# Kernel tuning notes

Measured on AMD Instinct MI355X. Metric: run time of the kernel, lower is better.

Reference implementation:

```python
import jax, jax.numpy as jnp
import numpy as np

N = 50000          # total nodes
E = 800000         # edges (avg degree 16)
IN = 128           # in_feat
HID = 64           # hidden per head
HEADS = (4, 4, 1)
NEG_SLOPE = 0.2    # DGL GATConv leaky_relu default


def setup_inputs() -> dict:
    key = jax.random.key(0)
    ks = jax.random.split(key, 16)

    def w(k, shape, fan_in):
        return jax.random.normal(k, shape, jnp.float32) / np.float32(np.sqrt(fan_in))

    inp = {
        "feat": jax.random.normal(ks[0], (N, IN), jnp.float32),
        "src": jax.random.randint(ks[1], (E,), 0, N, jnp.int32),
        "dst": jax.random.randint(ks[2], (E,), 0, N, jnp.int32),
    }
    dims = [(IN, HEADS[0]), (HID * HEADS[0], HEADS[1]), (HID * HEADS[1], HEADS[2])]
    j = 3
    for i, (din, h) in enumerate(dims, 1):
        inp[f"W{i}"] = w(ks[j], (din, h * HID), din); j += 1
        inp[f"al{i}"] = w(ks[j], (h, HID), HID); j += 1
        inp[f"ar{i}"] = w(ks[j], (h, HID), HID); j += 1
        inp[f"b{i}"] = jnp.zeros((h * HID,), jnp.float32)
    return inp


def gat_layer(x, W, al, ar, b, src, dst, n_heads):
    # DGL GATConv: linear -> per-node attn logits -> edge leaky_relu ->
    # per-dst segment softmax -> weighted scatter-sum -> + bias
    h = (x @ W).reshape(N, n_heads, HID)                     # [N,H,D]
    el = jnp.einsum("nhd,hd->nh", h, al)                     # [N,H]
    er = jnp.einsum("nhd,hd->nh", h, ar)                     # [N,H]
    e = jax.nn.leaky_relu(el[src] + er[dst], NEG_SLOPE)      # [E,H]
    m = jax.ops.segment_max(e, dst, num_segments=N)          # [N,H]
    m = jnp.where(jnp.isfinite(m), m, 0.0)                   # empty segments -> -inf
    ex = jnp.exp(e - m[dst])                                 # [E,H]
    s = jax.ops.segment_sum(ex, dst, num_segments=N)         # [N,H]
    alpha = ex / s[dst]                                      # [E,H]
    msg = h[src] * alpha[:, :, None]                         # [E,H,D]
    out = jax.ops.segment_sum(msg, dst, num_segments=N)      # [N,H,D]
    return out + b.reshape(1, n_heads, HID)


def reference(feat, src, dst, W1, al1, ar1, b1, W2, al2, ar2, b2, W3, al3, ar3, b3):
    h = jax.nn.elu(gat_layer(feat, W1, al1, ar1, b1, src, dst, HEADS[0]))
    h = h.reshape(N, HEADS[0] * HID)                         # flatten heads
    h = jax.nn.elu(gat_layer(h, W2, al2, ar2, b2, src, dst, HEADS[1]))
    h = h.reshape(N, HEADS[1] * HID)
    h = gat_layer(h, W3, al3, ar3, b3, src, dst, HEADS[2])   # no activation
    return h.mean(axis=1)                                    # [N, HID]
```

## Files before the change

### kernel.cpp

```cpp
#include <hip/hip_runtime.h>
#include <math.h>

#define HID 64
#define NSLOPE 0.2f
#define SB 512
#define EXCAP 256
#define BCAP 8192
#define OVFCAP 65536
#define NBK_MAX 256

typedef __attribute__((ext_vector_type(8))) short short8v;
typedef __attribute__((ext_vector_type(4))) float float4v;

__device__ inline unsigned short f2bf(float x) {
  unsigned u = __float_as_uint(x);
  u += 0x7fffu + ((u >> 16) & 1u);
  return (unsigned short)(u >> 16);
}
__device__ inline float bf2f(unsigned short h) {
  return __uint_as_float(((unsigned)h) << 16);
}
__device__ inline float bflo(unsigned u) { return __uint_as_float(u << 16); }
__device__ inline float bfhi(unsigned u) { return __uint_as_float(u & 0xffff0000u); }

__global__ __launch_bounds__(256) void k_split(const float* __restrict__ x,
    unsigned short* __restrict__ hi, unsigned short* __restrict__ lo, int n) {
  int i = blockIdx.x * 256 + threadIdx.x;
  if (i < n) {
    float v = x[i];
    unsigned short h = f2bf(v);
    hi[i] = h;
    lo[i] = f2bf(v - bf2f(h));
  }
}

__global__ __launch_bounds__(256) void k_wsplit(const float* __restrict__ W,
    unsigned short* __restrict__ Whi, unsigned short* __restrict__ Wlo, int K, int N) {
  int i = blockIdx.x * 256 + threadIdx.x;
  if (i < N * K) {
    int n = i / K, k = i - n * K;
    float v = W[(size_t)k * N + n];
    unsigned short h = f2bf(v);
    Whi[i] = h;
    Wlo[i] = f2bf(v - bf2f(h));
  }
}

__global__ __launch_bounds__(256) void gemm_split(
    const unsigned short* __restrict__ Ahi, const unsigned short* __restrict__ Alo,
    const unsigned short* __restrict__ Bhi, const unsigned short* __restrict__ Blo,
    float* __restrict__ C, unsigned short* __restrict__ Gp, int M, int Nc, int K, int H) {
  __shared__ __align__(16) unsigned short AsHi[128 * 40];
  __shared__ __align__(16) unsigned short AsLo[128 * 40];
  __shared__ __align__(16) unsigned short BsHi[128 * 40];
  __shared__ __align__(16) unsigned short BsLo[128 * 40];
  const int tid = threadIdx.x;
  const int lane = tid & 63, wid = tid >> 6;
  const int wr = wid >> 1, wc = wid & 1;
  const int row0 = blockIdx.y * 128;
  const int col0 = blockIdx.x * 128;
  float4v acc[4][4];
  #pragma unroll
  for (int mi = 0; mi < 4; ++mi)
    #pragma unroll
    for (int ni = 0; ni < 4; ++ni)
      acc[mi][ni] = (float4v){0.f, 0.f, 0.f, 0.f};

  const int sr = tid >> 2;
  const int sc8 = (tid & 3) * 8;
  const int lr = lane & 15, lk = (lane >> 4) * 8;

  for (int k0 = 0; k0 < K; k0 += 32) {
    #pragma unroll
    for (int half = 0; half < 2; ++half) {
      int row = sr + half * 64;
      int arow = row0 + row; if (arow > M - 1) arow = M - 1;
      int brow = col0 + row; if (brow > Nc - 1) brow = Nc - 1;
      *(short8v*)&AsHi[row * 40 + sc8] = *(const short8v*)&Ahi[(size_t)arow * K + k0 + sc8];
      *(short8v*)&AsLo[row * 40 + sc8] = *(const short8v*)&Alo[(size_t)arow * K + k0 + sc8];
      *(short8v*)&BsHi[row * 40 + sc8] = *(const short8v*)&Bhi[(size_t)brow * K + k0 + sc8];
      *(short8v*)&BsLo[row * 40 + sc8] = *(const short8v*)&Blo[(size_t)brow * K + k0 + sc8];
    }
    __syncthreads();
    short8v ah[4], alv[4], bh[4], bl[4];
    #pragma unroll
    for (int mi = 0; mi < 4; ++mi) {
      int r = wr * 64 + mi * 16 + lr;
      ah[mi]  = *(const short8v*)&AsHi[r * 40 + lk];
      alv[mi] = *(const short8v*)&AsLo[r * 40 + lk];
    }
    #pragma unroll
    for (int ni = 0; ni < 4; ++ni) {
      int r = wc * 64 + ni * 16 + lr;
      bh[ni] = *(const short8v*)&BsHi[r * 40 + lk];
      bl[ni] = *(const short8v*)&BsLo[r * 40 + lk];
    }
    #pragma unroll
    for (int mi = 0; mi < 4; ++mi)
      #pragma unroll
      for (int ni = 0; ni < 4; ++ni) {
        acc[mi][ni] = __builtin_amdgcn_mfma_f32_16x16x32_bf16(ah[mi], bh[ni], acc[mi][ni], 0, 0, 0);
        acc[mi][ni] = __builtin_amdgcn_mfma_f32_16x16x32_bf16(ah[mi], bl[ni], acc[mi][ni], 0, 0, 0);
        acc[mi][ni] = __builtin_amdgcn_mfma_f32_16x16x32_bf16(alv[mi], bh[ni], acc[mi][ni], 0, 0, 0);
      }
    __syncthreads();
  }
  #pragma unroll
  for (int mi = 0; mi < 4; ++mi) {
    int rbase = row0 + wr * 64 + mi * 16 + (lane >> 4) * 4;
    #pragma unroll
    for (int ni = 0; ni < 4; ++ni) {
      int cc = col0 + wc * 64 + ni * 16 + (lane & 15);
      if (cc < Nc) {
        int gcol = (cc & 63) * H + (cc >> 6);
        #pragma unroll
        for (int q = 0; q < 4; ++q) {
          int rr = rbase + q;
          if (rr < M) {
            float v = acc[mi][ni][q];
            C[(size_t)rr * Nc + cc] = v;
            Gp[(size_t)rr * Nc + gcol] = f2bf(v);
          }
        }
      }
    }
  }
}

__global__ __launch_bounds__(256) void elr_kernel(const float* __restrict__ h,
    const float* __restrict__ al, const float* __restrict__ ar,
    float* __restrict__ el, float* __restrict__ er, int H, int N) {
  int n = blockIdx.x * 4 + (threadIdx.x >> 6);
  int lane = threadIdx.x & 63;
  if (n >= N) return;
  const float* hr = h + (size_t)n * H * HID;
  for (int hh = 0; hh < H; ++hh) {
    float v = hr[hh * HID + lane];
    float a = v * al[hh * HID + lane];
    float b = v * ar[hh * HID + lane];
    #pragma unroll
    for (int o = 32; o > 0; o >>= 1) { a += __shfl_xor(a, o); b += __shfl_xor(b, o); }
    if (lane == 0) { el[n * H + hh] = a; er[n * H + hh] = b; }
  }
}

__global__ void k_count(const int* __restrict__ dst, int* __restrict__ deg, int E) {
  int e = blockIdx.x * blockDim.x + threadIdx.x;
  if (e < E) atomicAdd(&deg[dst[e]], 1);
}
__global__ __launch_bounds__(SB) void k_blocksums(const int* __restrict__ deg,
                                                  int* __restrict__ bsums, int n) {
  __shared__ int s[SB];
  int t = threadIdx.x, i = blockIdx.x * SB + t;
  s[t] = (i < n) ? deg[i] : 0;
  __syncthreads();
  for (int o = SB >> 1; o > 0; o >>= 1) { if (t < o) s[t] += s[t + o]; __syncthreads(); }
  if (t == 0) bsums[blockIdx.x] = s[0];
}
__global__ __launch_bounds__(SB) void k_scancarry(const int* __restrict__ bsums,
                                                   int* __restrict__ carry, int nb) {
  __shared__ int s[SB];
  int t = threadIdx.x;
  int v = (t < nb) ? bsums[t] : 0;
  s[t] = v; __syncthreads();
  for (int o = 1; o < SB; o <<= 1) {
    int u = (t >= o) ? s[t - o] : 0;
    __syncthreads(); s[t] += u; __syncthreads();
  }
  if (t < nb) carry[t] = s[t] - v;
}
__global__ __launch_bounds__(SB) void k_offsets(const int* __restrict__ deg,
    const int* __restrict__ carry, int* __restrict__ offs, int n, int E) {
  __shared__ int s[SB];
  int t = threadIdx.x, i = blockIdx.x * SB + t;
  int v = (i < n) ? deg[i] : 0;
  s[t] = v; __syncthreads();
  for (int o = 1; o < SB; o <<= 1) {
    int u = (t >= o) ? s[t - o] : 0;
    __syncthreads(); s[t] += u; __syncthreads();
  }
  if (i < n) offs[i] = carry[blockIdx.x] + s[t] - v;
  if (i == n) offs[n] = E;
}
__global__ __launch_bounds__(256) void k_binA(const int* __restrict__ src,
    const int* __restrict__ dst, int* __restrict__ bcur, unsigned* __restrict__ bbuf,
    unsigned* __restrict__ ovf, int* __restrict__ ovfcnt, int E, int nbk) {
  __shared__ int lcnt[NBK_MAX];
  __shared__ int lbase[NBK_MAX];
  const int tid = threadIdx.x;
  int per = (E + gridDim.x - 1) / gridDim.x;
  int e0 = blockIdx.x * per;
  int e1 = e0 + per; if (e1 > E) e1 = E;
  for (int b = tid; b < nbk; b += 256) lcnt[b] = 0;
  __syncthreads();
  for (int e = e0 + tid; e < e1; e += 256)
    atomicAdd(&lcnt[dst[e] >> 8], 1);
  __syncthreads();
  for (int b = tid; b < nbk; b += 256) {
    int c = lcnt[b];
    lbase[b] = (c > 0) ? atomicAdd(&bcur[b], c) : 0;
    lcnt[b] = 0;
  }
  __syncthreads();
  for (int e = e0 + tid; e < e1; e += 256) {
    int d = dst[e], s = src[e];
    int b = d >> 8;
    int pos = lbase[b] + atomicAdd(&lcnt[b], 1);
    unsigned packed = ((unsigned)d << 16) | (unsigned)s;
    if (pos < BCAP) {
      bbuf[(size_t)b * BCAP + pos] = packed;
    } else {
      int o = atomicAdd(ovfcnt, 1);
      if (o < OVFCAP) ovf[o] = packed;
    }
  }
}
__global__ __launch_bounds__(256) void k_binB(const int* __restrict__ bcur,
    const unsigned* __restrict__ bbuf, const int* __restrict__ offs,
    int* __restrict__ cursor, int* __restrict__ esrc, int N) {
  __shared__ int lcur[256];
  int b = blockIdx.x;
  int n0 = b << 8;
  int nn = N - n0; if (nn > 256) nn = 256;
  for (int i = threadIdx.x; i < 256; i += 256) lcur[i] = 0;
  __syncthreads();
  int cnt = bcur[b]; if (cnt > BCAP) cnt = BCAP;
  for (int i = threadIdx.x; i < cnt; i += 256) {
    unsigned v = bbuf[(size_t)b * BCAP + i];
    int d = (int)(v >> 16), s = (int)(v & 0xffffu);
    int slot = offs[d] + atomicAdd(&lcur[d & 255], 1);
    esrc[slot] = s;
  }
  __syncthreads();
  for (int i = threadIdx.x; i < nn; i += 256) cursor[n0 + i] = lcur[i];
}
__global__ __launch_bounds__(64) void k_ovf(const unsigned* __restrict__ ovf,
    const int* __restrict__ ovfcnt, const int* __restrict__ offs,
    int* __restrict__ cursor, int* __restrict__ esrc) {
  int cnt = *ovfcnt; if (cnt > OVFCAP) cnt = OVFCAP;
  for (int i = threadIdx.x; i < cnt; i += 64) {
    unsigned v = ovf[i];
    int d = (int)(v >> 16), s = (int)(v & 0xffffu);
    int slot = offs[d] + atomicAdd(&cursor[d], 1);
    esrc[slot] = s;
  }
}

template<int H, bool DO_ELU, bool SPLITOUT>
__global__ __launch_bounds__(64) void agg_kernel(const unsigned short* __restrict__ gp,
    const float* __restrict__ el, const float* __restrict__ er,
    const int* __restrict__ offs, const int* __restrict__ esrc,
    const float* __restrict__ bias,
    unsigned short* __restrict__ outHi, unsigned short* __restrict__ outLo,
    float* __restrict__ outF, int N) {
  constexpr int LPN = (H == 4) ? 32 : 16;
  constexpr int NPW = 64 / LPN;
  __shared__ __align__(16) float exs_all[NPW][EXCAP * H];
  const int lane = threadIdx.x;
  const int grp = lane / LPN;
  const int sl = lane % LPN;
  const int n = blockIdx.x * NPW + grp;
  if (n >= N) return;
  float* exs = exs_all[grp];
  const int off = offs[n];
  const int deg = offs[n + 1] - off;
  float ern[H];
  if (H == 4) {
    float4 R = *(const float4*)&er[n * 4];
    ern[0] = R.x; ern[1] = R.y; ern[2] = R.z; ern[3] = R.w;
  } else {
    ern[0] = er[n];
  }
  float sum[H];
  #pragma unroll
  for (int h = 0; h < H; ++h) sum[h] = 0.f;
  for (int base = 0; base < deg; base += LPN) {
    int i = base + sl;
    if (i < deg) {
      int s = esrc[off + i];
      if (H == 4) {
        float4 L = *(const float4*)&el[s * 4];
        float lv[4] = {L.x, L.y, L.z, L.w};
        float exv[4];
        #pragma unroll
        for (int h = 0; h < 4; ++h) {
          float e = lv[h] + ern[h];
          e = e > 0.f ? e : NSLOPE * e;
          exv[h] = __expf(fminf(e, 80.f));
          sum[h] += exv[h];
        }
        if (i < EXCAP)
          *(float4*)&exs[i * 4] = make_float4(exv[0], exv[1], exv[2], exv[3]);
      } else {
        float e = el[s] + ern[0];
        e = e > 0.f ? e : NSLOPE * e;
        float x = __expf(fminf(e, 80.f));
        sum[0] += x;
        if (i < EXCAP) exs[i] = x;
      }
    }
  }
  float inv[H];
  #pragma unroll
  for (int h = 0; h < H; ++h) {
    float v = sum[h];
    #pragma unroll
    for (int o = LPN / 2; o > 0; o >>= 1) v += __shfl_xor(v, o);
    inv[h] = v > 0.f ? 1.f / v : 0.f;
  }
  asm volatile("s_waitcnt lgkmcnt(0)" ::: "memory");
  const int degc = deg < EXCAP ? deg : EXCAP;
  int t = 0;
  if (H == 4) {
    float acc[8];
    #pragma unroll
    for (int k = 0; k < 8; ++k) acc[k] = 0.f;
    for (; t + 4 <= degc; t += 4) {
      int4 sa = *(const int4*)&esrc[off + t];
      int s[4] = {sa.x, sa.y, sa.z, sa.w};
      uint4 g[4];
      #pragma unroll
      for (int j = 0; j < 4; ++j)
        g[j] = *(const uint4*)&gp[(size_t)s[j] * 256 + sl * 8];
      #pragma unroll
      for (int j = 0; j < 4; ++j) {
        float4 x = *(const float4*)&exs[(t + j) * 4];
        acc[0] = fmaf(bflo(g[j].x), x.x, acc[0]);
        acc[1] = fmaf(bfhi(g[j].x), x.y, acc[1]);
        acc[2] = fmaf(bflo(g[j].y), x.z, acc[2]);
        acc[3] = fmaf(bfhi(g[j].y), x.w, acc[3]);
        acc[4] = fmaf(bflo(g[j].z), x.x, acc[4]);
        acc[5] = fmaf(bfhi(g[j].z), x.y, acc[5]);
        acc[6] = fmaf(bflo(g[j].w), x.z, acc[6]);
        acc[7] = fmaf(bfhi(g[j].w), x.w, acc[7]);
      }
    }
    for (; t < degc; ++t) {
      int s = esrc[off + t];
      uint4 g = *(const uint4*)&gp[(size_t)s * 256 + sl * 8];
      float4 x = *(const float4*)&exs[t * 4];
      acc[0] = fmaf(bflo(g.x), x.x, acc[0]);
      acc[1] = fmaf(bfhi(g.x), x.y, acc[1]);
      acc[2] = fmaf(bflo(g.y), x.z, acc[2]);
      acc[3] = fmaf(bfhi(g.y), x.w, acc[3]);
      acc[4] = fmaf(bflo(g.z), x.x, acc[4]);
      acc[5] = fmaf(bfhi(g.z), x.y, acc[5]);
      acc[6] = fmaf(bflo(g.w), x.z, acc[6]);
      acc[7] = fmaf(bfhi(g.w), x.w, acc[7]);
    }
    for (; t < deg; ++t) {
      int s = esrc[off + t];
      float4 L = *(const float4*)&el[s * 4];
      float lv[4] = {L.x, L.y, L.z, L.w};
      float xv[4];
      #pragma unroll
      for (int h = 0; h < 4; ++h) {
        float e = lv[h] + ern[h];
        e = e > 0.f ? e : NSLOPE * e;
        xv[h] = __expf(fminf(e, 80.f));
      }
      uint4 g = *(const uint4*)&gp[(size_t)s * 256 + sl * 8];
      acc[0] = fmaf(bflo(g.x), xv[0], acc[0]);
      acc[1] = fmaf(bfhi(g.x), xv[1], acc[1]);
      acc[2] = fmaf(bflo(g.y), xv[2], acc[2]);
      acc[3] = fmaf(bfhi(g.y), xv[3], acc[3]);
      acc[4] = fmaf(bflo(g.z), xv[0], acc[4]);
      acc[5] = fmaf(bfhi(g.z), xv[1], acc[5]);
      acc[6] = fmaf(bflo(g.w), xv[2], acc[6]);
      acc[7] = fmaf(bfhi(g.w), xv[3], acc[7]);
    }
    #pragma unroll
    for (int dd = 0; dd < 2; ++dd) {
      int d = 2 * sl + dd;
      #pragma unroll
      for (int hh = 0; hh < 4; ++hh) {
        float v = fmaf(acc[dd * 4 + hh], inv[hh], bias[hh * HID + d]);
        if (DO_ELU) v = v > 0.f ? v : expm1f(v);
        size_t oi = (size_t)n * 256 + hh * HID + d;
        if (SPLITOUT) {
          unsigned short hb = f2bf(v);
          outHi[oi] = hb;
          outLo[oi] = f2bf(v - bf2f(hb));
        } else {
          outF[oi] = v;
        }
      }
    }
  } else {
    float acc[4];
    #pragma unroll
    for (int k = 0; k < 4; ++k) acc[k] = 0.f;
    for (; t + 8 <= degc; t += 8) {
      int4 sa = *(const int4*)&esrc[off + t];
      int4 sb = *(const int4*)&esrc[off + t + 4];
      int s[8] = {sa.x, sa.y, sa.z, sa.w, sb.x, sb.y, sb.z, sb.w};
      uint2 g[8];
      #pragma unroll
      for (int j = 0; j < 8; ++j)
        g[j] = *(const uint2*)&gp[(size_t)s[j] * 64 + sl * 4];
      #pragma unroll
      for (int j = 0; j < 8; ++j) {
        float x = exs[t + j];
        acc[0] = fmaf(bflo(g[j].x), x, acc[0]);
        acc[1] = fmaf(bfhi(g[j].x), x, acc[1]);
        acc[2] = fmaf(bflo(g[j].y), x, acc[2]);
        acc[3] = fmaf(bfhi(g[j].y), x, acc[3]);
      }
    }
    for (; t < degc; ++t) {
      int s = esrc[off + t];
      uint2 g = *(const uint2*)&gp[(size_t)s * 64 + sl * 4];
      float x = exs[t];
      acc[0] = fmaf(bflo(g.x), x, acc[0]);
      acc[1] = fmaf(bfhi(g.x), x, acc[1]);
      acc[2] = fmaf(bflo(g.y), x, acc[2]);
      acc[3] = fmaf(bfhi(g.y), x, acc[3]);
    }
    for (; t < deg; ++t) {
      int s = esrc[off + t];
      float e = el[s] + ern[0];
      e = e > 0.f ? e : NSLOPE * e;
      float x = __expf(fminf(e, 80.f));
      uint2 g = *(const uint2*)&gp[(size_t)s * 64 + sl * 4];
      acc[0] = fmaf(bflo(g.x), x, acc[0]);
      acc[1] = fmaf(bfhi(g.x), x, acc[1]);
      acc[2] = fmaf(bflo(g.y), x, acc[2]);
      acc[3] = fmaf(bfhi(g.y), x, acc[3]);
    }
    #pragma unroll
    for (int k = 0; k < 4; ++k) {
      int d = 4 * sl + k;
      float v = fmaf(acc[k], inv[0], bias[d]);
      if (DO_ELU) v = v > 0.f ? v : expm1f(v);
      size_t oi = (size_t)n * HID + d;
      if (SPLITOUT) {
        unsigned short hb = f2bf(v);
        outHi[oi] = hb;
        outLo[oi] = f2bf(v - bf2f(hb));
      } else {
        outF[oi] = v;
      }
    }
  }
}

extern "C" void kernel_launch(void* const* d_in, const int* in_sizes, int n_in,
                              void* d_out, int out_size, void* d_ws, size_t ws_size,
                              hipStream_t stream) {
  const float* feat = (const float*)d_in[0];
  const int* src = (const int*)d_in[1];
  const int* dst = (const int*)d_in[2];
  const float* W1 = (const float*)d_in[3];
  const float* al1 = (const float*)d_in[4];
  const float* ar1 = (const float*)d_in[5];
  const float* b1 = (const float*)d_in[6];
  const float* W2 = (const float*)d_in[7];
  const float* al2 = (const float*)d_in[8];
  const float* ar2 = (const float*)d_in[9];
  const float* b2 = (const float*)d_in[10];
  const float* W3 = (const float*)d_in[11];
  const float* al3 = (const float*)d_in[12];
  const float* ar3 = (const float*)d_in[13];
  const float* b3 = (const float*)d_in[14];
  const int N = in_sizes[0] / 128;
  const int E = in_sizes[1];

  char* w = (char*)d_ws;
  auto alloc = [&](size_t bytes) {
    void* p = (void*)w;
    w += (bytes + 255) & ~(size_t)255;
    return p;
  };
  unsigned short* pHi = (unsigned short*)alloc((size_t)N * 256 * 2);
  unsigned short* pLo = (unsigned short*)alloc((size_t)N * 256 * 2);
  float* Cbuf = (float*)alloc((size_t)N * 256 * 4);
  unsigned short* Gp = (unsigned short*)alloc((size_t)N * 256 * 2);
  float* el = (float*)alloc((size_t)N * 4 * 4);
  float* er = (float*)alloc((size_t)N * 4 * 4);
  int* deg = (int*)alloc((size_t)N * 4);
  int* cursor = (int*)alloc((size_t)N * 4);
  int* offs = (int*)alloc((size_t)(N + 1) * 4);
  int nb = (N + SB - 1) / SB;
  int* bsums = (int*)alloc((size_t)nb * 4);
  int* carry = (int*)alloc((size_t)nb * 4);
  int* esrc = (int*)alloc((size_t)E * 4);
  int nbk = (N + 255) >> 8;
  int* bcur = (int*)alloc((size_t)nbk * 4);
  unsigned* bbuf = (unsigned*)alloc((size_t)nbk * BCAP * 4);
  unsigned* ovf = (unsigned*)alloc((size_t)OVFCAP * 4);
  int* ovfcnt = (int*)alloc(256);
  unsigned short* W1h = (unsigned short*)alloc((size_t)256 * 128 * 2);
  unsigned short* W1l = (unsigned short*)alloc((size_t)256 * 128 * 2);
  unsigned short* W2h = (unsigned short*)alloc((size_t)256 * 256 * 2);
  unsigned short* W2l = (unsigned short*)alloc((size_t)256 * 256 * 2);
  unsigned short* W3h = (unsigned short*)alloc((size_t)64 * 256 * 2);
  unsigned short* W3l = (unsigned short*)alloc((size_t)64 * 256 * 2);

  hipMemsetAsync(deg, 0, (size_t)N * 4, stream);
  hipMemsetAsync(bcur, 0, (size_t)nbk * 4, stream);
  hipMemsetAsync(ovfcnt, 0, 256, stream);
  int eb = (E + 255) / 256;
  k_count<<<eb, 256, 0, stream>>>(dst, deg, E);
  k_blocksums<<<nb, SB, 0, stream>>>(deg, bsums, N);
  k_scancarry<<<1, SB, 0, stream>>>(bsums, carry, nb);
  k_offsets<<<nb, SB, 0, stream>>>(deg, carry, offs, N, E);
  k_binA<<<256, 256, 0, stream>>>(src, dst, bcur, bbuf, ovf, ovfcnt, E, nbk);
  k_binB<<<nbk, 256, 0, stream>>>(bcur, bbuf, offs, cursor, esrc, N);
  k_ovf<<<1, 64, 0, stream>>>(ovf, ovfcnt, offs, cursor, esrc);

  k_wsplit<<<(256 * 128 + 255) / 256, 256, 0, stream>>>(W1, W1h, W1l, 128, 256);
  k_wsplit<<<(256 * 256 + 255) / 256, 256, 0, stream>>>(W2, W2h, W2l, 256, 256);
  k_wsplit<<<(64 * 256 + 255) / 256, 256, 0, stream>>>(W3, W3h, W3l, 256, 64);

  k_split<<<((N * 128) + 255) / 256, 256, 0, stream>>>(feat, pHi, pLo, N * 128);

  int rg = (N + 127) / 128;
  int ng4 = (N + 3) / 4;
  int ag4 = (N + 1) / 2;
  int ag1 = (N + 3) / 4;
  gemm_split<<<dim3(2, rg), 256, 0, stream>>>(pHi, pLo, W1h, W1l, Cbuf, Gp, N, 256, 128, 4);
  elr_kernel<<<ng4, 256, 0, stream>>>(Cbuf, al1, ar1, el, er, 4, N);
  agg_kernel<4, true, true><<<ag4, 64, 0, stream>>>(Gp, el, er, offs, esrc, b1, pHi, pLo, nullptr, N);
  gemm_split<<<dim3(2, rg), 256, 0, stream>>>(pHi, pLo, W2h, W2l, Cbuf, Gp, N, 256, 256, 4);
  elr_kernel<<<ng4, 256, 0, stream>>>(Cbuf, al2, ar2, el, er, 4, N);
  agg_kernel<4, true, true><<<ag4, 64, 0, stream>>>(Gp, el, er, offs, esrc, b2, pHi, pLo, nullptr, N);
  gemm_split<<<dim3(1, rg), 256, 0, stream>>>(pHi, pLo, W3h, W3l, Cbuf, Gp, N, 64, 256, 1);
  elr_kernel<<<ng4, 256, 0, stream>>>(Cbuf, al3, ar3, el, er, 1, N);
  agg_kernel<1, false, false><<<ag1, 64, 0, stream>>>(Gp, el, er, offs, esrc, b3, nullptr, nullptr, (float*)d_out, N);
}
```

Baseline: 443.4 us.

## Fold attention vectors into weights and drop fp32 GEMM output buffer

Precomputes W·al and W·ar per layer so the attention logits el/er come straight from the layer input rather than from the fp32 projected features. The GEMM then only writes the bf16 gathered buffer, which removes the large fp32 C store and the elr kernel that read it back. Degree counting is also moved to come from the binned edge buffer with shared-memory atomics instead of global atomics over all edges. The cost is slightly different rounding in the logits and a few small extra prep kernels.

```diff
diff --git a/kernel.cpp b/kernel.cpp
--- a/kernel.cpp
+++ b/kernel.cpp
@@ -46,10 +46,88 @@
   }
 }
 
+__global__ __launch_bounds__(256) void k_walprep(const float* __restrict__ W,
+    const float* __restrict__ al, const float* __restrict__ ar,
+    float* __restrict__ Wal, int K, int Nc, int H) {
+  int k = blockIdx.x * 256 + threadIdx.x;
+  if (k >= K) return;
+  for (int j = 0; j < H; ++j) {
+    float sl = 0.f, sr = 0.f;
+    for (int d = 0; d < HID; ++d) {
+      float wv = W[(size_t)k * Nc + j * HID + d];
+      sl = fmaf(wv, al[j * HID + d], sl);
+      sr = fmaf(wv, ar[j * HID + d], sr);
+    }
+    Wal[(size_t)k * 2 * H + j] = sl;
+    Wal[(size_t)k * 2 * H + H + j] = sr;
+  }
+}
+
+__global__ __launch_bounds__(256) void k_elr_f32(const float* __restrict__ x,
+    const float* __restrict__ Wal, float* __restrict__ el, float* __restrict__ er, int N) {
+  int n = blockIdx.x * 4 + (threadIdx.x >> 6);
+  int lane = threadIdx.x & 63;
+  if (n >= N) return;
+  float2 xv = *(const float2*)&x[(size_t)n * 128 + lane * 2];
+  float p[8];
+  #pragma unroll
+  for (int j = 0; j < 8; ++j) p[j] = 0.f;
+  #pragma unroll
+  for (int kk = 0; kk < 2; ++kk) {
+    float xk = (kk == 0) ? xv.x : xv.y;
+    const float* wr = &Wal[(size_t)(lane * 2 + kk) * 8];
+    float4 wa = *(const float4*)wr;
+    float4 wb = *(const float4*)(wr + 4);
+    p[0] = fmaf(xk, wa.x, p[0]); p[1] = fmaf(xk, wa.y, p[1]);
+    p[2] = fmaf(xk, wa.z, p[2]); p[3] = fmaf(xk, wa.w, p[3]);
+    p[4] = fmaf(xk, wb.x, p[4]); p[5] = fmaf(xk, wb.y, p[5]);
+    p[6] = fmaf(xk, wb.z, p[6]); p[7] = fmaf(xk, wb.w, p[7]);
+  }
+  #pragma unroll
+  for (int j = 0; j < 8; ++j)
+    #pragma unroll
+    for (int o = 32; o > 0; o >>= 1) p[j] += __shfl_xor(p[j], o);
+  if (lane == 0) {
+    *(float4*)&el[n * 4] = make_float4(p[0], p[1], p[2], p[3]);
+    *(float4*)&er[n * 4] = make_float4(p[4], p[5], p[6], p[7]);
+  }
+}
+
+template<int H>
+__global__ __launch_bounds__(256) void k_elr_bf(const unsigned short* __restrict__ xhi,
+    const unsigned short* __restrict__ xlo, const float* __restrict__ Wal,
+    float* __restrict__ el, float* __restrict__ er, int N) {
+  constexpr int NJ = 2 * H;
+  int n = blockIdx.x * 4 + (threadIdx.x >> 6);
+  int lane = threadIdx.x & 63;
+  if (n >= N) return;
+  uint2 hv = *(const uint2*)&xhi[(size_t)n * 256 + lane * 4];
+  uint2 lv = *(const uint2*)&xlo[(size_t)n * 256 + lane * 4];
+  float x[4] = { bflo(hv.x) + bflo(lv.x), bfhi(hv.x) + bfhi(lv.x),
+                 bflo(hv.y) + bflo(lv.y), bfhi(hv.y) + bfhi(lv.y) };
+  float p[NJ];
+  #pragma unroll
+  for (int j = 0; j < NJ; ++j) p[j] = 0.f;
+  #pragma unroll
+  for (int kk = 0; kk < 4; ++kk) {
+    const float* wr = &Wal[(size_t)(lane * 4 + kk) * NJ];
+    #pragma unroll
+    for (int j = 0; j < NJ; ++j) p[j] = fmaf(x[kk], wr[j], p[j]);
+  }
+  #pragma unroll
+  for (int j = 0; j < NJ; ++j)
+    #pragma unroll
+    for (int o = 32; o > 0; o >>= 1) p[j] += __shfl_xor(p[j], o);
+  if (lane == 0) {
+    #pragma unroll
+    for (int j = 0; j < H; ++j) { el[n * H + j] = p[j]; er[n * H + j] = p[H + j]; }
+  }
+}
+
 __global__ __launch_bounds__(256) void gemm_split(
     const unsigned short* __restrict__ Ahi, const unsigned short* __restrict__ Alo,
     const unsigned short* __restrict__ Bhi, const unsigned short* __restrict__ Blo,
-    float* __restrict__ C, unsigned short* __restrict__ Gp, int M, int Nc, int K, int H) {
+    unsigned short* __restrict__ Gp, int M, int Nc, int K, int H) {
   __shared__ __align__(16) unsigned short AsHi[128 * 40];
   __shared__ __align__(16) unsigned short AsLo[128 * 40];
   __shared__ __align__(16) unsigned short BsHi[128 * 40];
@@ -116,38 +194,13 @@
         #pragma unroll
         for (int q = 0; q < 4; ++q) {
           int rr = rbase + q;
-          if (rr < M) {
-            float v = acc[mi][ni][q];
-            C[(size_t)rr * Nc + cc] = v;
-            Gp[(size_t)rr * Nc + gcol] = f2bf(v);
-          }
+          if (rr < M) Gp[(size_t)rr * Nc + gcol] = f2bf(acc[mi][ni][q]);
         }
       }
     }
   }
 }
 
-__global__ __launch_bounds__(256) void elr_kernel(const float* __restrict__ h,
-    const float* __restrict__ al, const float* __restrict__ ar,
-    float* __restrict__ el, float* __restrict__ er, int H, int N) {
-  int n = blockIdx.x * 4 + (threadIdx.x >> 6);
-  int lane = threadIdx.x & 63;
-  if (n >= N) return;
-  const float* hr = h + (size_t)n * H * HID;
-  for (int hh = 0; hh < H; ++hh) {
-    float v = hr[hh * HID + lane];
-    float a = v * al[hh * HID + lane];
-    float b = v * ar[hh * HID + lane];
-    #pragma unroll
-    for (int o = 32; o > 0; o >>= 1) { a += __shfl_xor(a, o); b += __shfl_xor(b, o); }
-    if (lane == 0) { el[n * H + hh] = a; er[n * H + hh] = b; }
-  }
-}
-
-__global__ void k_count(const int* __restrict__ dst, int* __restrict__ deg, int E) {
-  int e = blockIdx.x * blockDim.x + threadIdx.x;
-  if (e < E) atomicAdd(&deg[dst[e]], 1);
-}
 __global__ __launch_bounds__(SB) void k_blocksums(const int* __restrict__ deg,
                                                   int* __restrict__ bsums, int n) {
   __shared__ int s[SB];
@@ -215,6 +268,25 @@
     }
   }
 }
+__global__ __launch_bounds__(256) void k_degB(const int* __restrict__ bcur,
+    const unsigned* __restrict__ bbuf, int* __restrict__ deg, int N) {
+  __shared__ int lcnt[256];
+  int b = blockIdx.x;
+  lcnt[threadIdx.x] = 0;
+  __syncthreads();
+  int cnt = bcur[b]; if (cnt > BCAP) cnt = BCAP;
+  for (int i = threadIdx.x; i < cnt; i += 256)
+    atomicAdd(&lcnt[(bbuf[(size_t)b * BCAP + i] >> 16) & 255], 1);
+  __syncthreads();
+  int n0 = b << 8;
+  if (n0 + threadIdx.x < N) deg[n0 + threadIdx.x] = lcnt[threadIdx.x];
+}
+__global__ __launch_bounds__(64) void k_degovf(const unsigned* __restrict__ ovf,
+    const int* __restrict__ ovfcnt, int* __restrict__ deg) {
+  int cnt = *ovfcnt; if (cnt > OVFCAP) cnt = OVFCAP;
+  for (int i = threadIdx.x; i < cnt; i += 64)
+    atomicAdd(&deg[(int)(ovf[i] >> 16)], 1);
+}
 __global__ __launch_bounds__(256) void k_binB(const int* __restrict__ bcur,
     const unsigned* __restrict__ bbuf, const int* __restrict__ offs,
     int* __restrict__ cursor, int* __restrict__ esrc, int N) {
@@ -222,7 +294,7 @@
   int b = blockIdx.x;
   int n0 = b << 8;
   int nn = N - n0; if (nn > 256) nn = 256;
-  for (int i = threadIdx.x; i < 256; i += 256) lcur[i] = 0;
+  lcur[threadIdx.x] = 0;
   __syncthreads();
   int cnt = bcur[b]; if (cnt > BCAP) cnt = BCAP;
   for (int i = threadIdx.x; i < cnt; i += 256) {
@@ -232,7 +304,7 @@
     esrc[slot] = s;
   }
   __syncthreads();
-  for (int i = threadIdx.x; i < nn; i += 256) cursor[n0 + i] = lcur[i];
+  if (threadIdx.x < nn) cursor[n0 + threadIdx.x] = lcur[threadIdx.x];
 }
 __global__ __launch_bounds__(64) void k_ovf(const unsigned* __restrict__ ovf,
     const int* __restrict__ ovfcnt, const int* __restrict__ offs,
@@ -473,7 +545,6 @@
   };
   unsigned short* pHi = (unsigned short*)alloc((size_t)N * 256 * 2);
   unsigned short* pLo = (unsigned short*)alloc((size_t)N * 256 * 2);
-  float* Cbuf = (float*)alloc((size_t)N * 256 * 4);
   unsigned short* Gp = (unsigned short*)alloc((size_t)N * 256 * 2);
   float* el = (float*)alloc((size_t)N * 4 * 4);
   float* er = (float*)alloc((size_t)N * 4 * 4);
@@ -495,22 +566,27 @@
   unsigned short* W2l = (unsigned short*)alloc((size_t)256 * 256 * 2);
   unsigned short* W3h = (unsigned short*)alloc((size_t)64 * 256 * 2);
   unsigned short* W3l = (unsigned short*)alloc((size_t)64 * 256 * 2);
-
-  hipMemsetAsync(deg, 0, (size_t)N * 4, stream);
+  float* Wal1 = (float*)alloc((size_t)128 * 8 * 4);
+  float* Wal2 = (float*)alloc((size_t)256 * 8 * 4);
+  float* Wal3 = (float*)alloc((size_t)256 * 2 * 4);
+
   hipMemsetAsync(bcur, 0, (size_t)nbk * 4, stream);
   hipMemsetAsync(ovfcnt, 0, 256, stream);
-  int eb = (E + 255) / 256;
-  k_count<<<eb, 256, 0, stream>>>(dst, deg, E);
+  k_binA<<<256, 256, 0, stream>>>(src, dst, bcur, bbuf, ovf, ovfcnt, E, nbk);
+  k_degB<<<nbk, 256, 0, stream>>>(bcur, bbuf, deg, N);
+  k_degovf<<<1, 64, 0, stream>>>(ovf, ovfcnt, deg);
   k_blocksums<<<nb, SB, 0, stream>>>(deg, bsums, N);
   k_scancarry<<<1, SB, 0, stream>>>(bsums, carry, nb);
   k_offsets<<<nb, SB, 0, stream>>>(deg, carry, offs, N, E);
-  k_binA<<<256, 256, 0, stream>>>(src, dst, bcur, bbuf, ovf, ovfcnt, E, nbk);
   k_binB<<<nbk, 256, 0, stream>>>(bcur, bbuf, offs, cursor, esrc, N);
   k_ovf<<<1, 64, 0, stream>>>(ovf, ovfcnt, offs, cursor, esrc);
 
   k_wsplit<<<(256 * 128 + 255) / 256, 256, 0, stream>>>(W1, W1h, W1l, 128, 256);
   k_wsplit<<<(256 * 256 + 255) / 256, 256, 0, stream>>>(W2, W2h, W2l, 256, 256);
   k_wsplit<<<(64 * 256 + 255) / 256, 256, 0, stream>>>(W3, W3h, W3l, 256, 64);
+  k_walprep<<<1, 256, 0, stream>>>(W1, al1, ar1, Wal1, 128, 256, 4);
+  k_walprep<<<1, 256, 0, stream>>>(W2, al2, ar2, Wal2, 256, 256, 4);
+  k_walprep<<<1, 256, 0, stream>>>(W3, al3, ar3, Wal3, 256, 64, 1);
 
   k_split<<<((N * 128) + 255) / 256, 256, 0, stream>>>(feat, pHi, pLo, N * 128);
 
@@ -518,13 +594,13 @@
   int ng4 = (N + 3) / 4;
   int ag4 = (N + 1) / 2;
   int ag1 = (N + 3) / 4;
-  gemm_split<<<dim3(2, rg), 256, 0, stream>>>(pHi, pLo, W1h, W1l, Cbuf, Gp, N, 256, 128, 4);
-  elr_kernel<<<ng4, 256, 0, stream>>>(Cbuf, al1, ar1, el, er, 4, N);
+  k_elr_f32<<<ng4, 256, 0, stream>>>(feat, Wal1, el, er, N);
+  gemm_split<<<dim3(2, rg), 256, 0, stream>>>(pHi, pLo, W1h, W1l, Gp, N, 256, 128, 4);
   agg_kernel<4, true, true><<<ag4, 64, 0, stream>>>(Gp, el, er, offs, esrc, b1, pHi, pLo, nullptr, N);
-  gemm_split<<<dim3(2, rg), 256, 0, stream>>>(pHi, pLo, W2h, W2l, Cbuf, Gp, N, 256, 256, 4);
-  elr_kernel<<<ng4, 256, 0, stream>>>(Cbuf, al2, ar2, el, er, 4, N);
+  k_elr_bf<4><<<ng4, 256, 0, stream>>>(pHi, pLo, Wal2, el, er, N);
+  gemm_split<<<dim3(2, rg), 256, 0, stream>>>(pHi, pLo, W2h, W2l, Gp, N, 256, 256, 4);
   agg_kernel<4, true, true><<<ag4, 64, 0, stream>>>(Gp, el, er, offs, esrc, b2, pHi, pLo, nullptr, N);
-  gemm_split<<<dim3(1, rg), 256, 0, stream>>>(pHi, pLo, W3h, W3l, Cbuf, Gp, N, 64, 256, 1);
-  elr_kernel<<<ng4, 256, 0, stream>>>(Cbuf, al3, ar3, el, er, 1, N);
+  k_elr_bf<1><<<ng4, 256, 0, stream>>>(pHi, pLo, Wal3, el, er, N);
+  gemm_split<<<dim3(1, rg), 256, 0, stream>>>(pHi, pLo, W3h, W3l, Gp, N, 64, 256, 1);
   agg_kernel<1, false, false><<<ag1, 64, 0, stream>>>(Gp, el, er, offs, esrc, b3, nullptr, nullptr, (float*)d_out, N);
 }
```

After: 437.8 us. About the same (-1.3%).
